# Performance work log

Hardware: AMD Instinct MI355X
Metric: run time of the kernel (lower is better)

The kernel has to match this reference:

```python
import jax, jax.numpy as jnp
import numpy as np

HIGH_THRESHOLD = 0.1
EPS = 1e-6


def _gaussian_kernel_2d(ksize=5, sigma=1.0):
    x = np.arange(ksize, dtype=np.float32) - ksize // 2
    g = np.exp(-(x * x) / (2.0 * sigma * sigma))
    g = g / g.sum()
    return (g[:, None] * g[None, :]).astype(np.float32)  # (5,5)


def _sobel_kernels():
    gx = np.array([[-1.0, 0.0, 1.0], [-2.0, 0.0, 2.0], [-1.0, 0.0, 1.0]], np.float32)
    gy = gx.T.copy()
    return np.stack([gx, gy])[:, None]  # (2,1,3,3)


def _nms_kernels():
    # kornia get_canny_nms_kernel: 8 direction kernels, center 1, -1 at neighbor
    k = np.zeros((8, 1, 3, 3), np.float32)
    k[:, 0, 1, 1] = 1.0
    offs = [(1, 2), (0, 2), (0, 1), (0, 0), (1, 0), (2, 0), (2, 1), (2, 2)]
    for i, (r, c) in enumerate(offs):
        k[i, 0, r, c] = -1.0
    return k


def _conv(x, w, pad, mode=None):
    # x: (B,Cin,H,W), w: (Cout,Cin,kh,kw)
    if mode is not None:
        x = jnp.pad(x, ((0, 0), (0, 0), (pad, pad), (pad, pad)), mode=mode)
        padding = 'VALID'
    else:
        padding = [(pad, pad), (pad, pad)]
    return jax.lax.conv_general_dilated(
        x, w, (1, 1), padding, dimension_numbers=('NCHW', 'OIHW', 'NCHW'))


def cal_edge(x):
    dt = x.dtype
    if x.shape[1] == 3:  # rgb_to_grayscale
        w = jnp.array([0.299, 0.587, 0.114], dt).reshape(1, 3, 1, 1)
        x = jnp.sum(x * w, axis=1, keepdims=True)
    # gaussian_blur2d, reflect border (kornia default)
    blurred = _conv(x, jnp.asarray(_gaussian_kernel_2d())[None, None], 2, mode='reflect')
    # spatial_gradient (sobel, replicate border)
    grads = _conv(blurred, jnp.asarray(_sobel_kernels()), 1, mode='edge')  # (B,2,H,W)
    gx, gy = grads[:, 0:1], grads[:, 1:2]
    magnitude = jnp.sqrt(gx * gx + gy * gy + EPS)  # (B,1,H,W)
    angle = jnp.arctan2(gy, gx) * (180.0 / np.pi)
    angle = jnp.round(angle / 45.0) * 45.0
    nms_mag = _conv(magnitude, jnp.asarray(_nms_kernels()), 1)  # (B,8,H,W), zero pad
    pos_idx = jnp.mod(angle / 45.0, 8.0).astype(jnp.int32)        # (B,1,H,W)
    neg_idx = jnp.mod(angle / 45.0 + 4.0, 8.0).astype(jnp.int32)
    cp = jnp.take_along_axis(nms_mag, pos_idx, axis=1)
    cn = jnp.take_along_axis(nms_mag, neg_idx, axis=1)
    is_max = jnp.minimum(cp, cn) > 0.0
    magnitude = magnitude * is_max
    # F.threshold(mag, high, 0); then F.threshold(-e, -high, -1); e = -e
    e1 = jnp.where(magnitude > HIGH_THRESHOLD, magnitude, jnp.zeros((), dt))
    edges = -jnp.where(-e1 > -HIGH_THRESHOLD, -e1, jnp.full((), -1.0, dt))
    return edges


def setup_inputs() -> dict:
    key = jax.random.key(0)
    k1, k2 = jax.random.split(key)
    shape = (8, 3, 1024, 1024)
    op = jax.random.uniform(k1, shape, jnp.float32)
    gt = jax.random.uniform(k2, shape, jnp.float32)
    return {'op': op, 'gt': gt}


def reference(op, gt):
    edge_op = cal_edge(op)
    edge_gt = cal_edge(gt)
    return jnp.mean(jnp.abs(edge_op - edge_gt))
```

## Files before the change

### kernel.cpp

```cpp
#include <hip/hip_runtime.h>

#define N 1024
#define NN (N * N)
#define STRIPS 9
#define SEGS 64
#define SEGROWS 16
#define NWAVES (STRIPS * SEGS * 8)

__device__ __forceinline__ int refl(int i) {
    if (i < 0) return -i;
    if (i >= N) return 2 * N - 2 - i;
    return i;
}
__device__ __forceinline__ float shl(float v, int sl) { return __shfl(v, sl, 64); }

struct F2 { float x, y; };

__device__ __forceinline__ int axcode(float gx, float gy) {
    float ax = fabsf(gx), ay = fabsf(gy);
    return (ay <= 0.41421356f * ax) ? 0
         : (ay >= 2.41421356f * ax) ? 1
         : (((gx > 0.f) == (gy > 0.f)) ? 2 : 3);
}

__device__ __forceinline__ float pick(int code, float r, float u, float ur, float ul) {
    return code == 0 ? r : code == 1 ? u : code == 2 ? ur : ul;
}

template<bool EC>
__device__ __forceinline__ int strip_body(const float* __restrict__ A,
                                          const float* __restrict__ B,
                                          int cb, int R0, int lane)
{
    const float w0 = 0.05448868f, w1 = 0.24420134f, w2 = 0.40261996f,
                w3 = 0.24420134f, w4 = 0.05448868f;
    const int c0 = cb + 2 * lane, c1 = c0 + 1;
    const int lm = lane - 1, lp = lane + 1;
    const int cR0 = refl(c0), cR1 = refl(c1);
    const bool p0 = (c0 == 0);
    const bool pN = (c1 == N - 1);
    const bool v0 = (lane >= 2 && lane <= 61 && c0 >= 0 && c0 < N);
    const bool v1 = (lane >= 2 && lane <= 61 && c1 < N);

    F2 ha0{},ha1{},ha2{},ha3{},ha4{}, hb0{},hb1{},hb2{},hb3{},hb4{};
    F2 bla0{},bla1{},bla2{}, blb0{},blb1{},blb2{};
    F2 mga0{},mga1{},mga2{}, mgla0{},mgla1{},mgla2{}, mgra0{},mgra1{},mgra2{};
    F2 mgb0{},mgb1{},mgb2{}, mglb0{},mglb1{},mglb2{}, mgrb0{},mgrb1{},mgrb2{};
    int axax = 0, axay = 0, axbx = 0, axby = 0;

    int acc = 0;

#pragma unroll 4
    for (int y = R0 - 4; y <= R0 + SEGROWS + 3; ++y) {
        const int rr = refl(y);
        F2 ga, gb;
        if (EC) {
            const float* pa0 = A + (size_t)rr * N + cR0;
            const float* pa1 = A + (size_t)rr * N + cR1;
            const float* pb0 = B + (size_t)rr * N + cR0;
            const float* pb1 = B + (size_t)rr * N + cR1;
            ga.x = 0.299f*pa0[0] + 0.587f*pa0[NN] + 0.114f*pa0[2*NN];
            ga.y = 0.299f*pa1[0] + 0.587f*pa1[NN] + 0.114f*pa1[2*NN];
            gb.x = 0.299f*pb0[0] + 0.587f*pb0[NN] + 0.114f*pb0[2*NN];
            gb.y = 0.299f*pb1[0] + 0.587f*pb1[NN] + 0.114f*pb1[2*NN];
        } else {
            const float* pa = A + (size_t)rr * N + c0;
            const float* pb = B + (size_t)rr * N + c0;
            float2 r  = *(const float2*)pa;
            float2 g  = *(const float2*)(pa + NN);
            float2 bb = *(const float2*)(pa + 2 * NN);
            ga.x = 0.299f*r.x + 0.587f*g.x + 0.114f*bb.x;
            ga.y = 0.299f*r.y + 0.587f*g.y + 0.114f*bb.y;
            r  = *(const float2*)pb;
            g  = *(const float2*)(pb + NN);
            bb = *(const float2*)(pb + 2 * NN);
            gb.x = 0.299f*r.x + 0.587f*g.x + 0.114f*bb.x;
            gb.y = 0.299f*r.y + 0.587f*g.y + 0.114f*bb.y;
        }

        float gaLx = shl(ga.x, lm), gaLy = shl(ga.y, lm);
        float gaRx = shl(ga.x, lp), gaRy = shl(ga.y, lp);
        float gbLx = shl(gb.x, lm), gbLy = shl(gb.y, lm);
        float gbRx = shl(gb.x, lp), gbRy = shl(gb.y, lp);
        F2 hna, hnb;
        hna.x = w0*gaLx + w1*gaLy + w2*ga.x + w3*ga.y + w4*gaRx;
        hna.y = w0*gaLy + w1*ga.x + w2*ga.y + w3*gaRx + w4*gaRy;
        hnb.x = w0*gbLx + w1*gbLy + w2*gb.x + w3*gb.y + w4*gbRx;
        hnb.y = w0*gbLy + w1*gb.x + w2*gb.y + w3*gbRx + w4*gbRy;
        ha0=ha1; ha1=ha2; ha2=ha3; ha3=ha4; ha4=hna;
        hb0=hb1; hb1=hb2; hb2=hb3; hb3=hb4; hb4=hnb;

        F2 bna, bnb;
        bna.x = w0*ha0.x + w1*ha1.x + w2*ha2.x + w3*ha3.x + w4*ha4.x;
        bna.y = w0*ha0.y + w1*ha1.y + w2*ha2.y + w3*ha3.y + w4*ha4.y;
        bnb.x = w0*hb0.x + w1*hb1.x + w2*hb2.x + w3*hb3.x + w4*hb4.x;
        bnb.y = w0*hb0.y + w1*hb1.y + w2*hb2.y + w3*hb3.y + w4*hb4.y;
        bla0=bla1; bla1=bla2; bla2=bna;
        blb0=blb1; blb1=blb2; blb2=bnb;

        const int z = y - 3;
        F2 bA0 = bla0, bA2 = bla2, bB0 = blb0, bB2 = blb2;
        if (z == 0)     { bA0 = bla1; bB0 = blb1; }
        if (z == N - 1) { bA2 = bla1; bB2 = blb1; }
        F2 sa, da, sb, db;
        sa.x = bA0.x + 2.f*bla1.x + bA2.x;  sa.y = bA0.y + 2.f*bla1.y + bA2.y;
        da.x = bA2.x - bA0.x;               da.y = bA2.y - bA0.y;
        sb.x = bB0.x + 2.f*blb1.x + bB2.x;  sb.y = bB0.y + 2.f*blb1.y + bB2.y;
        db.x = bB2.x - bB0.x;               db.y = bB2.y - bB0.y;

        float saLy = shl(sa.y, lm), saRx = shl(sa.x, lp);
        float daLy = shl(da.y, lm), daRx = shl(da.x, lp);
        float sbLy = shl(sb.y, lm), sbRx = shl(sb.x, lp);
        float dbLy = shl(db.y, lm), dbRx = shl(db.x, lp);
        if (EC) {
            saLy = p0 ? sa.x : saLy;  daLy = p0 ? da.x : daLy;
            sbLy = p0 ? sb.x : sbLy;  dbLy = p0 ? db.x : dbLy;
            saRx = pN ? sa.y : saRx;  daRx = pN ? da.y : daRx;
            sbRx = pN ? sb.y : sbRx;  dbRx = pN ? db.y : dbRx;
        }
        F2 gxa, gya, gxb, gyb;
        gxa.x = sa.y - saLy;              gxa.y = saRx - sa.x;
        gya.x = daLy + 2.f*da.x + da.y;   gya.y = da.x + 2.f*da.y + daRx;
        gxb.x = sb.y - sbLy;              gxb.y = sbRx - sb.x;
        gyb.x = dbLy + 2.f*db.x + db.y;   gyb.y = db.x + 2.f*db.y + dbRx;

        F2 maga, magb;
        maga.x = sqrtf(gxa.x*gxa.x + gya.x*gya.x + 1e-6f);
        maga.y = sqrtf(gxa.y*gxa.y + gya.y*gya.y + 1e-6f);
        magb.x = sqrtf(gxb.x*gxb.x + gyb.x*gyb.x + 1e-6f);
        magb.y = sqrtf(gxb.y*gxb.y + gyb.y*gyb.y + 1e-6f);

        int cax = axcode(gxa.x, gya.x), cay = axcode(gxa.y, gya.y);
        int cbx = axcode(gxb.x, gyb.x), cby = axcode(gxb.y, gyb.y);

        float maLy = shl(maga.y, lm), maRx = shl(maga.x, lp);
        float mbLy = shl(magb.y, lm), mbRx = shl(magb.x, lp);
        if (EC) {
            maLy = p0 ? 0.f : maLy;  mbLy = p0 ? 0.f : mbLy;
            maRx = pN ? 0.f : maRx;  mbRx = pN ? 0.f : mbRx;
        }
        F2 mla{maLy, maga.x}, mra{maga.y, maRx};
        F2 mlb{mbLy, magb.x}, mrb{magb.y, mbRx};

        mga0=mga1;   mga1=mga2;   mga2=maga;
        mgla0=mgla1; mgla1=mgla2; mgla2=mla;
        mgra0=mgra1; mgra1=mgra2; mgra2=mra;
        mgb0=mgb1;   mgb1=mgb2;   mgb2=magb;
        mglb0=mglb1; mglb1=mglb2; mglb2=mlb;
        mgrb0=mgrb1; mgrb1=mgrb2; mgrb2=mrb;

        const int axUax = axax, axUay = axay, axUbx = axbx, axUby = axby;
        axax = cax; axay = cay; axbx = cbx; axby = cby;

        if (y >= R0 + 4) {
            const int w = y - 4;
            F2 upA=mga0, upLA=mgla0, upRA=mgra0, dnA=mga2, dnLA=mgla2, dnRA=mgra2;
            F2 upB=mgb0, upLB=mglb0, upRB=mgrb0, dnB=mgb2, dnLB=mglb2, dnRB=mgrb2;
            if (w == 0) {
                upA = F2{0,0}; upLA = F2{0,0}; upRA = F2{0,0};
                upB = F2{0,0}; upLB = F2{0,0}; upRB = F2{0,0};
            }
            if (w == N - 1) {
                dnA = F2{0,0}; dnLA = F2{0,0}; dnRA = F2{0,0};
                dnB = F2{0,0}; dnLB = F2{0,0}; dnRB = F2{0,0};
            }
            float n1ax = pick(axUax, mgra1.x, upA.x, upRA.x, upLA.x);
            float n2ax = pick(axUax, mgla1.x, dnA.x, dnLA.x, dnRA.x);
            float n1ay = pick(axUay, mgra1.y, upA.y, upRA.y, upLA.y);
            float n2ay = pick(axUay, mgla1.y, dnA.y, dnLA.y, dnRA.y);
            float n1bx = pick(axUbx, mgrb1.x, upB.x, upRB.x, upLB.x);
            float n2bx = pick(axUbx, mglb1.x, dnB.x, dnLB.x, dnRB.x);
            float n1by = pick(axUby, mgrb1.y, upB.y, upRB.y, upLB.y);
            float n2by = pick(axUby, mglb1.y, dnB.y, dnLB.y, dnRB.y);
            bool eax = (mga1.x > n1ax) && (mga1.x > n2ax) && (mga1.x > 0.1f);
            bool eay = (mga1.y > n1ay) && (mga1.y > n2ay) && (mga1.y > 0.1f);
            bool ebx = (mgb1.x > n1bx) && (mgb1.x > n2bx) && (mgb1.x > 0.1f);
            bool eby = (mgb1.y > n1by) && (mgb1.y > n2by) && (mgb1.y > 0.1f);
            acc += (int)(v0 && (eax != ebx));
            acc += (int)(v1 && (eay != eby));
        }
    }
    return acc;
}

__global__ __launch_bounds__(64)
void edge_diff_kernel(const float* __restrict__ op, const float* __restrict__ gt,
                      unsigned int* __restrict__ partials)
{
    int b = blockIdx.x;
    int img   = b / (STRIPS * SEGS);
    int rem   = b - img * (STRIPS * SEGS);
    int strip = rem / SEGS;
    int seg   = rem - strip * SEGS;
    int lane  = threadIdx.x;

    int cb = strip * 120 - 4;
    int R0 = seg * SEGROWS;
    const float* A = op + (size_t)img * 3 * NN;
    const float* B = gt + (size_t)img * 3 * NN;

    int acc;
    if (strip == 0 || strip == STRIPS - 1)
        acc = strip_body<true>(A, B, cb, R0, lane);
    else
        acc = strip_body<false>(A, B, cb, R0, lane);

    for (int off = 32; off > 0; off >>= 1)
        acc += __shfl_down(acc, off, 64);
    if (lane == 0) partials[b] = (unsigned int)acc;
}

__global__ __launch_bounds__(256)
void finalize_kernel(const unsigned int* __restrict__ partials, float* __restrict__ out)
{
    __shared__ unsigned int ws[4];
    int tid = threadIdx.x;
    unsigned int sum = 0;
    for (int i = tid; i < NWAVES; i += 256)
        sum += partials[i];
    int d = (int)sum;
    for (int off = 32; off > 0; off >>= 1)
        d += __shfl_down(d, off, 64);
    if ((tid & 63) == 0) ws[tid >> 6] = (unsigned int)d;
    __syncthreads();
    if (tid == 0)
        out[0] = (float)(ws[0] + ws[1] + ws[2] + ws[3]) / 8388608.0f;
}

extern "C" void kernel_launch(void* const* d_in, const int* in_sizes, int n_in,
                              void* d_out, int out_size, void* d_ws, size_t ws_size,
                              hipStream_t stream)
{
    const float* op = (const float*)d_in[0];
    const float* gt = (const float*)d_in[1];
    unsigned int* partials = (unsigned int*)d_ws;

    edge_diff_kernel<<<dim3(NWAVES), dim3(64), 0, stream>>>(op, gt, partials);
    finalize_kernel<<<1, dim3(256), 0, stream>>>(partials, (float*)d_out);
}
```

Before: 246.2 us.

## Halve segment height, pack four waves per block, peel pipeline warm-up

Segments shrink from 16 to 8 rows, doubling the wave count, and waves are grouped four per 256-thread block with a launch-bounds occupancy hint. The stencil pipeline is split into helper steps, and the warm-up rows are peeled into separate loops so the main loop no longer branches on whether output is ready. The aim is more parallelism and occupancy, but the halo overhead per segment grows from 8 extra rows over 16 to 8 over 8, which adds redundant loads and compute.

```diff
diff --git a/kernel.cpp b/kernel.cpp
--- a/kernel.cpp
+++ b/kernel.cpp
@@ -3,9 +3,11 @@
 #define N 1024
 #define NN (N * N)
 #define STRIPS 9
-#define SEGS 64
-#define SEGROWS 16
+#define SEGS 128
+#define SEGROWS 8
+#define WPB 4
 #define NWAVES (STRIPS * SEGS * 8)
+#define NBLOCKS (NWAVES / WPB)
 
 __device__ __forceinline__ int refl(int i) {
     if (i < 0) return -i;
@@ -22,18 +24,111 @@
          : (ay >= 2.41421356f * ax) ? 1
          : (((gx > 0.f) == (gy > 0.f)) ? 2 : 3);
 }
-
 __device__ __forceinline__ float pick(int code, float r, float u, float ur, float ul) {
     return code == 0 ? r : code == 1 ? u : code == 2 ? ur : ul;
 }
 
+#define W0 0.05448868f
+#define W1 0.24420134f
+#define W2 0.40261996f
+#define W3 0.24420134f
+#define W4 0.05448868f
+
+struct St {
+    F2 h0, h1, h2, h3, h4;
+    F2 bl0, bl1, bl2;
+    F2 mg0, mg1, mg2;
+    F2 ml0, ml1, ml2;
+    F2 mr0, mr1, mr2;
+    int ax_x, ax_y;
+    int axp_x, axp_y;
+};
+
 template<bool EC>
-__device__ __forceinline__ int strip_body(const float* __restrict__ A,
-                                          const float* __restrict__ B,
-                                          int cb, int R0, int lane)
-{
-    const float w0 = 0.05448868f, w1 = 0.24420134f, w2 = 0.40261996f,
-                w3 = 0.24420134f, w4 = 0.05448868f;
+__device__ __forceinline__ F2 gray_load(const float* __restrict__ I, int rr,
+                                        int c0, int cR0, int cR1)
+{
+    F2 g;
+    if (EC) {
+        const float* q0 = I + (size_t)rr * N + cR0;
+        const float* q1 = I + (size_t)rr * N + cR1;
+        g.x = 0.299f*q0[0] + 0.587f*q0[NN] + 0.114f*q0[2*NN];
+        g.y = 0.299f*q1[0] + 0.587f*q1[NN] + 0.114f*q1[2*NN];
+    } else {
+        const float* p = I + (size_t)rr * N + c0;
+        float2 r  = *(const float2*)p;
+        float2 gg = *(const float2*)(p + NN);
+        float2 bb = *(const float2*)(p + 2 * NN);
+        g.x = 0.299f*r.x + 0.587f*gg.x + 0.114f*bb.x;
+        g.y = 0.299f*r.y + 0.587f*gg.y + 0.114f*bb.y;
+    }
+    return g;
+}
+
+__device__ __forceinline__ void step_h(St& s, F2 g, int lm, int lp) {
+    float gLx = shl(g.x, lm), gLy = shl(g.y, lm);
+    float gRx = shl(g.x, lp), gRy = shl(g.y, lp);
+    F2 hn;
+    hn.x = W0*gLx + W1*gLy + W2*g.x + W3*g.y + W4*gRx;
+    hn.y = W0*gLy + W1*g.x + W2*g.y + W3*gRx + W4*gRy;
+    s.h0 = s.h1; s.h1 = s.h2; s.h2 = s.h3; s.h3 = s.h4; s.h4 = hn;
+}
+
+__device__ __forceinline__ void step_v(St& s) {
+    F2 bn;
+    bn.x = W0*s.h0.x + W1*s.h1.x + W2*s.h2.x + W3*s.h3.x + W4*s.h4.x;
+    bn.y = W0*s.h0.y + W1*s.h1.y + W2*s.h2.y + W3*s.h3.y + W4*s.h4.y;
+    s.bl0 = s.bl1; s.bl1 = s.bl2; s.bl2 = bn;
+}
+
+template<bool EC>
+__device__ __forceinline__ void step_sobel(St& s, bool zT, bool zB,
+                                           int lm, int lp, bool p0, bool pN)
+{
+    F2 b0 = zT ? s.bl1 : s.bl0;
+    F2 b2 = zB ? s.bl1 : s.bl2;
+    F2 sa, da;
+    sa.x = b0.x + 2.f*s.bl1.x + b2.x;  sa.y = b0.y + 2.f*s.bl1.y + b2.y;
+    da.x = b2.x - b0.x;                da.y = b2.y - b0.y;
+    float sLy = shl(sa.y, lm), sRx = shl(sa.x, lp);
+    float dLy = shl(da.y, lm), dRx = shl(da.x, lp);
+    if (EC) {
+        sLy = p0 ? sa.x : sLy;  dLy = p0 ? da.x : dLy;
+        sRx = pN ? sa.y : sRx;  dRx = pN ? da.y : dRx;
+    }
+    F2 gx, gy;
+    gx.x = sa.y - sLy;               gx.y = sRx - sa.x;
+    gy.x = dLy + 2.f*da.x + da.y;    gy.y = da.x + 2.f*da.y + dRx;
+    F2 mag;
+    mag.x = sqrtf(gx.x*gx.x + gy.x*gy.x + 1e-6f);
+    mag.y = sqrtf(gx.y*gx.y + gy.y*gy.y + 1e-6f);
+    s.axp_x = s.ax_x;  s.axp_y = s.ax_y;
+    s.ax_x = axcode(gx.x, gy.x);  s.ax_y = axcode(gx.y, gy.y);
+    float mLy = shl(mag.y, lm), mRx = shl(mag.x, lp);
+    if (EC) { mLy = p0 ? 0.f : mLy;  mRx = pN ? 0.f : mRx; }
+    s.mg0 = s.mg1; s.mg1 = s.mg2; s.mg2 = mag;
+    s.ml0 = s.ml1; s.ml1 = s.ml2; s.ml2 = F2{mLy, mag.x};
+    s.mr0 = s.mr1; s.mr1 = s.mr2; s.mr2 = F2{mag.y, mRx};
+}
+
+__device__ __forceinline__ void nms(const St& s, bool wT, bool wB, bool& ex, bool& ey) {
+    F2 up = s.mg0, upL = s.ml0, upR = s.mr0;
+    F2 dn = s.mg2, dnL = s.ml2, dnR = s.mr2;
+    if (wT) { up = F2{0,0}; upL = F2{0,0}; upR = F2{0,0}; }
+    if (wB) { dn = F2{0,0}; dnL = F2{0,0}; dnR = F2{0,0}; }
+    float n1x = pick(s.axp_x, s.mr1.x, up.x, upR.x, upL.x);
+    float n2x = pick(s.axp_x, s.ml1.x, dn.x, dnL.x, dnR.x);
+    float n1y = pick(s.axp_y, s.mr1.y, up.y, upR.y, upL.y);
+    float n2y = pick(s.axp_y, s.ml1.y, dn.y, dnL.y, dnR.y);
+    ex = (s.mg1.x > n1x) && (s.mg1.x > n2x) && (s.mg1.x > 0.1f);
+    ey = (s.mg1.y > n1y) && (s.mg1.y > n2y) && (s.mg1.y > 0.1f);
+}
+
+template<bool EC>
+__device__ __forceinline__ int strip_seg(const float* __restrict__ A,
+                                         const float* __restrict__ B,
+                                         int cb, int R0, int lane)
+{
     const int c0 = cb + 2 * lane, c1 = c0 + 1;
     const int lm = lane - 1, lp = lane + 1;
     const int cR0 = refl(c0), cR1 = refl(c1);
@@ -42,157 +137,62 @@
     const bool v0 = (lane >= 2 && lane <= 61 && c0 >= 0 && c0 < N);
     const bool v1 = (lane >= 2 && lane <= 61 && c1 < N);
 
-    F2 ha0{},ha1{},ha2{},ha3{},ha4{}, hb0{},hb1{},hb2{},hb3{},hb4{};
-    F2 bla0{},bla1{},bla2{}, blb0{},blb1{},blb2{};
-    F2 mga0{},mga1{},mga2{}, mgla0{},mgla1{},mgla2{}, mgra0{},mgra1{},mgra2{};
-    F2 mgb0{},mgb1{},mgb2{}, mglb0{},mglb1{},mglb2{}, mgrb0{},mgrb1{},mgrb2{};
-    int axax = 0, axay = 0, axbx = 0, axby = 0;
-
+    St sA{}, sB{};
     int acc = 0;
 
+#pragma unroll
+    for (int k = 0; k < 4; ++k) {
+        int rr = refl(R0 - 4 + k);
+        step_h(sA, gray_load<EC>(A, rr, c0, cR0, cR1), lm, lp);
+        step_h(sB, gray_load<EC>(B, rr, c0, cR0, cR1), lm, lp);
+    }
+#pragma unroll
+    for (int k = 0; k < 2; ++k) {
+        int rr = refl(R0 + k);
+        step_h(sA, gray_load<EC>(A, rr, c0, cR0, cR1), lm, lp);  step_v(sA);
+        step_h(sB, gray_load<EC>(B, rr, c0, cR0, cR1), lm, lp);  step_v(sB);
+    }
+#pragma unroll
+    for (int k = 0; k < 2; ++k) {
+        int y = R0 + 2 + k;
+        int rr = refl(y);
+        int z = y - 3;
+        bool zT = (z == 0), zB = (z == N - 1);
+        step_h(sA, gray_load<EC>(A, rr, c0, cR0, cR1), lm, lp);
+        step_v(sA);  step_sobel<EC>(sA, zT, zB, lm, lp, p0, pN);
+        step_h(sB, gray_load<EC>(B, rr, c0, cR0, cR1), lm, lp);
+        step_v(sB);  step_sobel<EC>(sB, zT, zB, lm, lp, p0, pN);
+    }
 #pragma unroll 4
-    for (int y = R0 - 4; y <= R0 + SEGROWS + 3; ++y) {
-        const int rr = refl(y);
-        F2 ga, gb;
-        if (EC) {
-            const float* pa0 = A + (size_t)rr * N + cR0;
-            const float* pa1 = A + (size_t)rr * N + cR1;
-            const float* pb0 = B + (size_t)rr * N + cR0;
-            const float* pb1 = B + (size_t)rr * N + cR1;
-            ga.x = 0.299f*pa0[0] + 0.587f*pa0[NN] + 0.114f*pa0[2*NN];
-            ga.y = 0.299f*pa1[0] + 0.587f*pa1[NN] + 0.114f*pa1[2*NN];
-            gb.x = 0.299f*pb0[0] + 0.587f*pb0[NN] + 0.114f*pb0[2*NN];
-            gb.y = 0.299f*pb1[0] + 0.587f*pb1[NN] + 0.114f*pb1[2*NN];
-        } else {
-            const float* pa = A + (size_t)rr * N + c0;
-            const float* pb = B + (size_t)rr * N + c0;
-            float2 r  = *(const float2*)pa;
-            float2 g  = *(const float2*)(pa + NN);
-            float2 bb = *(const float2*)(pa + 2 * NN);
-            ga.x = 0.299f*r.x + 0.587f*g.x + 0.114f*bb.x;
-            ga.y = 0.299f*r.y + 0.587f*g.y + 0.114f*bb.y;
-            r  = *(const float2*)pb;
-            g  = *(const float2*)(pb + NN);
-            bb = *(const float2*)(pb + 2 * NN);
-            gb.x = 0.299f*r.x + 0.587f*g.x + 0.114f*bb.x;
-            gb.y = 0.299f*r.y + 0.587f*g.y + 0.114f*bb.y;
-        }
-
-        float gaLx = shl(ga.x, lm), gaLy = shl(ga.y, lm);
-        float gaRx = shl(ga.x, lp), gaRy = shl(ga.y, lp);
-        float gbLx = shl(gb.x, lm), gbLy = shl(gb.y, lm);
-        float gbRx = shl(gb.x, lp), gbRy = shl(gb.y, lp);
-        F2 hna, hnb;
-        hna.x = w0*gaLx + w1*gaLy + w2*ga.x + w3*ga.y + w4*gaRx;
-        hna.y = w0*gaLy + w1*ga.x + w2*ga.y + w3*gaRx + w4*gaRy;
-        hnb.x = w0*gbLx + w1*gbLy + w2*gb.x + w3*gb.y + w4*gbRx;
-        hnb.y = w0*gbLy + w1*gb.x + w2*gb.y + w3*gbRx + w4*gbRy;
-        ha0=ha1; ha1=ha2; ha2=ha3; ha3=ha4; ha4=hna;
-        hb0=hb1; hb1=hb2; hb2=hb3; hb3=hb4; hb4=hnb;
-
-        F2 bna, bnb;
-        bna.x = w0*ha0.x + w1*ha1.x + w2*ha2.x + w3*ha3.x + w4*ha4.x;
-        bna.y = w0*ha0.y + w1*ha1.y + w2*ha2.y + w3*ha3.y + w4*ha4.y;
-        bnb.x = w0*hb0.x + w1*hb1.x + w2*hb2.x + w3*hb3.x + w4*hb4.x;
-        bnb.y = w0*hb0.y + w1*hb1.y + w2*hb2.y + w3*hb3.y + w4*hb4.y;
-        bla0=bla1; bla1=bla2; bla2=bna;
-        blb0=blb1; blb1=blb2; blb2=bnb;
-
-        const int z = y - 3;
-        F2 bA0 = bla0, bA2 = bla2, bB0 = blb0, bB2 = blb2;
-        if (z == 0)     { bA0 = bla1; bB0 = blb1; }
-        if (z == N - 1) { bA2 = bla1; bB2 = blb1; }
-        F2 sa, da, sb, db;
-        sa.x = bA0.x + 2.f*bla1.x + bA2.x;  sa.y = bA0.y + 2.f*bla1.y + bA2.y;
-        da.x = bA2.x - bA0.x;               da.y = bA2.y - bA0.y;
-        sb.x = bB0.x + 2.f*blb1.x + bB2.x;  sb.y = bB0.y + 2.f*blb1.y + bB2.y;
-        db.x = bB2.x - bB0.x;               db.y = bB2.y - bB0.y;
-
-        float saLy = shl(sa.y, lm), saRx = shl(sa.x, lp);
-        float daLy = shl(da.y, lm), daRx = shl(da.x, lp);
-        float sbLy = shl(sb.y, lm), sbRx = shl(sb.x, lp);
-        float dbLy = shl(db.y, lm), dbRx = shl(db.x, lp);
-        if (EC) {
-            saLy = p0 ? sa.x : saLy;  daLy = p0 ? da.x : daLy;
-            sbLy = p0 ? sb.x : sbLy;  dbLy = p0 ? db.x : dbLy;
-            saRx = pN ? sa.y : saRx;  daRx = pN ? da.y : daRx;
-            sbRx = pN ? sb.y : sbRx;  dbRx = pN ? db.y : dbRx;
-        }
-        F2 gxa, gya, gxb, gyb;
-        gxa.x = sa.y - saLy;              gxa.y = saRx - sa.x;
-        gya.x = daLy + 2.f*da.x + da.y;   gya.y = da.x + 2.f*da.y + daRx;
-        gxb.x = sb.y - sbLy;              gxb.y = sbRx - sb.x;
-        gyb.x = dbLy + 2.f*db.x + db.y;   gyb.y = db.x + 2.f*db.y + dbRx;
-
-        F2 maga, magb;
-        maga.x = sqrtf(gxa.x*gxa.x + gya.x*gya.x + 1e-6f);
-        maga.y = sqrtf(gxa.y*gxa.y + gya.y*gya.y + 1e-6f);
-        magb.x = sqrtf(gxb.x*gxb.x + gyb.x*gyb.x + 1e-6f);
-        magb.y = sqrtf(gxb.y*gxb.y + gyb.y*gyb.y + 1e-6f);
-
-        int cax = axcode(gxa.x, gya.x), cay = axcode(gxa.y, gya.y);
-        int cbx = axcode(gxb.x, gyb.x), cby = axcode(gxb.y, gyb.y);
-
-        float maLy = shl(maga.y, lm), maRx = shl(maga.x, lp);
-        float mbLy = shl(magb.y, lm), mbRx = shl(magb.x, lp);
-        if (EC) {
-            maLy = p0 ? 0.f : maLy;  mbLy = p0 ? 0.f : mbLy;
-            maRx = pN ? 0.f : maRx;  mbRx = pN ? 0.f : mbRx;
-        }
-        F2 mla{maLy, maga.x}, mra{maga.y, maRx};
-        F2 mlb{mbLy, magb.x}, mrb{magb.y, mbRx};
-
-        mga0=mga1;   mga1=mga2;   mga2=maga;
-        mgla0=mgla1; mgla1=mgla2; mgla2=mla;
-        mgra0=mgra1; mgra1=mgra2; mgra2=mra;
-        mgb0=mgb1;   mgb1=mgb2;   mgb2=magb;
-        mglb0=mglb1; mglb1=mglb2; mglb2=mlb;
-        mgrb0=mgrb1; mgrb1=mgrb2; mgrb2=mrb;
-
-        const int axUax = axax, axUay = axay, axUbx = axbx, axUby = axby;
-        axax = cax; axay = cay; axbx = cbx; axby = cby;
-
-        if (y >= R0 + 4) {
-            const int w = y - 4;
-            F2 upA=mga0, upLA=mgla0, upRA=mgra0, dnA=mga2, dnLA=mgla2, dnRA=mgra2;
-            F2 upB=mgb0, upLB=mglb0, upRB=mgrb0, dnB=mgb2, dnLB=mglb2, dnRB=mgrb2;
-            if (w == 0) {
-                upA = F2{0,0}; upLA = F2{0,0}; upRA = F2{0,0};
-                upB = F2{0,0}; upLB = F2{0,0}; upRB = F2{0,0};
-            }
-            if (w == N - 1) {
-                dnA = F2{0,0}; dnLA = F2{0,0}; dnRA = F2{0,0};
-                dnB = F2{0,0}; dnLB = F2{0,0}; dnRB = F2{0,0};
-            }
-            float n1ax = pick(axUax, mgra1.x, upA.x, upRA.x, upLA.x);
-            float n2ax = pick(axUax, mgla1.x, dnA.x, dnLA.x, dnRA.x);
-            float n1ay = pick(axUay, mgra1.y, upA.y, upRA.y, upLA.y);
-            float n2ay = pick(axUay, mgla1.y, dnA.y, dnLA.y, dnRA.y);
-            float n1bx = pick(axUbx, mgrb1.x, upB.x, upRB.x, upLB.x);
-            float n2bx = pick(axUbx, mglb1.x, dnB.x, dnLB.x, dnRB.x);
-            float n1by = pick(axUby, mgrb1.y, upB.y, upRB.y, upLB.y);
-            float n2by = pick(axUby, mglb1.y, dnB.y, dnLB.y, dnRB.y);
-            bool eax = (mga1.x > n1ax) && (mga1.x > n2ax) && (mga1.x > 0.1f);
-            bool eay = (mga1.y > n1ay) && (mga1.y > n2ay) && (mga1.y > 0.1f);
-            bool ebx = (mgb1.x > n1bx) && (mgb1.x > n2bx) && (mgb1.x > 0.1f);
-            bool eby = (mgb1.y > n1by) && (mgb1.y > n2by) && (mgb1.y > 0.1f);
-            acc += (int)(v0 && (eax != ebx));
-            acc += (int)(v1 && (eay != eby));
-        }
+    for (int k = 0; k < SEGROWS; ++k) {
+        int y = R0 + 4 + k;
+        int rr = refl(y);
+        int z = y - 3, w = y - 4;
+        bool zT = (z == 0), zB = (z == N - 1);
+        bool wT = (w == 0), wB = (w == N - 1);
+        step_h(sA, gray_load<EC>(A, rr, c0, cR0, cR1), lm, lp);
+        step_v(sA);  step_sobel<EC>(sA, zT, zB, lm, lp, p0, pN);
+        step_h(sB, gray_load<EC>(B, rr, c0, cR0, cR1), lm, lp);
+        step_v(sB);  step_sobel<EC>(sB, zT, zB, lm, lp, p0, pN);
+        bool eax, eay, ebx, eby;
+        nms(sA, wT, wB, eax, eay);
+        nms(sB, wT, wB, ebx, eby);
+        acc += (int)(v0 && (eax != ebx));
+        acc += (int)(v1 && (eay != eby));
     }
     return acc;
 }
 
-__global__ __launch_bounds__(64)
+__global__ __launch_bounds__(256, 8)
 void edge_diff_kernel(const float* __restrict__ op, const float* __restrict__ gt,
                       unsigned int* __restrict__ partials)
 {
-    int b = blockIdx.x;
-    int img   = b / (STRIPS * SEGS);
-    int rem   = b - img * (STRIPS * SEGS);
+    int lane  = threadIdx.x & 63;
+    int gwave = blockIdx.x * WPB + (threadIdx.x >> 6);
+    int img   = gwave / (STRIPS * SEGS);
+    int rem   = gwave - img * (STRIPS * SEGS);
     int strip = rem / SEGS;
     int seg   = rem - strip * SEGS;
-    int lane  = threadIdx.x;
 
     int cb = strip * 120 - 4;
     int R0 = seg * SEGROWS;
@@ -201,13 +201,13 @@
 
     int acc;
     if (strip == 0 || strip == STRIPS - 1)
-        acc = strip_body<true>(A, B, cb, R0, lane);
+        acc = strip_seg<true>(A, B, cb, R0, lane);
     else
-        acc = strip_body<false>(A, B, cb, R0, lane);
+        acc = strip_seg<false>(A, B, cb, R0, lane);
 
     for (int off = 32; off > 0; off >>= 1)
         acc += __shfl_down(acc, off, 64);
-    if (lane == 0) partials[b] = (unsigned int)acc;
+    if (lane == 0) partials[gwave] = (unsigned int)acc;
 }
 
 __global__ __launch_bounds__(256)
@@ -235,6 +235,6 @@
     const float* gt = (const float*)d_in[1];
     unsigned int* partials = (unsigned int*)d_ws;
 
-    edge_diff_kernel<<<dim3(NWAVES), dim3(64), 0, stream>>>(op, gt, partials);
+    edge_diff_kernel<<<dim3(NBLOCKS), dim3(256), 0, stream>>>(op, gt, partials);
     finalize_kernel<<<1, dim3(256), 0, stream>>>(partials, (float*)d_out);
 }
```

Result: slower. 498.2 us (+102.4%).
